# Performance work log

Measured on AMD Instinct MI355X. Metric: run time of the kernel, lower is better.

## Reference

```python
import jax, jax.numpy as jnp
import numpy as np

B, S, DIM, HEADS, MLP = 2, 2048, 1024, 16, 4096
DH = DIM // HEADS
LN_EPS = 1e-5


def layernorm(x, g, b):
    m = x.mean(-1, keepdims=True)
    v = ((x - m) ** 2).mean(-1, keepdims=True)
    return (x - m) / jnp.sqrt(v + LN_EPS) * g + b


def rope(x):
    # x: [B, H, S, dh]; interleaved-pair RoPE (rotary_embedding_torch convention)
    dh = x.shape[-1]
    s = x.shape[-2]
    inv_freq = 1.0 / (10000.0 ** (jnp.arange(0, dh, 2, dtype=jnp.float32) / dh))
    freqs = jnp.arange(s, dtype=jnp.float32)[:, None] * inv_freq[None, :]  # [S, dh/2]
    cos = jnp.repeat(jnp.cos(freqs), 2, axis=-1)  # [S, dh]
    sin = jnp.repeat(jnp.sin(freqs), 2, axis=-1)
    xp = x.reshape(x.shape[:-1] + (dh // 2, 2))
    x_rot = jnp.stack([-xp[..., 1], xp[..., 0]], axis=-1).reshape(x.shape)
    return x * cos + x_rot * sin


def setup_inputs() -> dict:
    key = jax.random.key(0)
    ks = jax.random.split(key, 10)
    w = 0.02
    return {
        "x": jax.random.normal(ks[0], (B, S, DIM), jnp.float32),
        "bias": jax.random.normal(ks[1], (B, S, S), jnp.float32) * 0.1,
        "ln1_g": jnp.ones((DIM,), jnp.float32),
        "ln1_b": jnp.zeros((DIM,), jnp.float32),
        "W_qkv": jax.random.normal(ks[2], (DIM, 3 * DIM), jnp.float32) * w,
        "W_o": jax.random.normal(ks[3], (DIM, DIM), jnp.float32) * w,
        "ln2_g": jnp.ones((DIM,), jnp.float32),
        "ln2_b": jnp.zeros((DIM,), jnp.float32),
        "W1": jax.random.normal(ks[4], (DIM, MLP), jnp.float32) * w,
        "b1": jnp.zeros((MLP,), jnp.float32),
        "W2": jax.random.normal(ks[5], (MLP, DIM), jnp.float32) * w,
        "b2": jnp.zeros((DIM,), jnp.float32),
        "pad_mask": jnp.zeros((B, S), jnp.int32),
    }


def reference(x, bias, ln1_g, ln1_b, W_qkv, W_o, ln2_g, ln2_b, W1, b1, W2, b2, pad_mask):
    b, s, d = x.shape
    h, dh = HEADS, DH
    res = x
    x1 = layernorm(x, ln1_g, ln1_b)
    qkv = (x1 @ W_qkv).reshape(b, s, h, 3 * dh)
    q, k, v = jnp.split(qkv, 3, axis=-1)            # each [B,S,H,dh]
    q = rope(q.transpose(0, 2, 1, 3))               # [B,H,S,dh]
    k = rope(k.transpose(0, 2, 1, 3))
    v = v.transpose(0, 2, 1, 3)
    scores = jnp.einsum("bhqd,bhkd->bhqk", q, k) * (dh ** -0.5)
    scores = scores + bias[:, None]                 # additive bias per batch
    key_mask = pad_mask.astype(bool)[:, None, None, :]
    scores = jnp.where(key_mask, -jnp.inf, scores)
    attn = jax.nn.softmax(scores, axis=-1)          # dropout = identity (eval)
    out = jnp.einsum("bhqk,bhkd->bhqd", attn, v)
    out = out.transpose(0, 2, 1, 3).reshape(b, s, d)
    x = res + out @ W_o
    res2 = x
    x2 = layernorm(x, ln2_g, ln2_b)
    mlp = jax.nn.gelu(x2 @ W1 + b1, approximate=False) @ W2 + b2
    return res2 + mlp
```

## Files before the change

### kernel.cpp

```cpp
#include <hip/hip_runtime.h>
#include <hip/hip_bf16.h>

#define B_   2
#define S_   2048
#define DIM_ 1024
#define H_   16
#define DH_  64
#define MLP_ 4096

typedef __bf16 bf16x8 __attribute__((ext_vector_type(8)));
typedef float  f32x4  __attribute__((ext_vector_type(4)));

__device__ __forceinline__ ushort f2bf(float f) {
    __bf16 h = (__bf16)f;
    return __builtin_bit_cast(ushort, h);
}
__device__ __forceinline__ float bf2f(ushort b) {
    union { unsigned u; float f; } x; x.u = ((unsigned)b) << 16;
    return x.f;
}

#define GLOAD_LDS16(gptr, lptr)                                                        \
    __builtin_amdgcn_global_load_lds(                                                  \
        (const __attribute__((address_space(1))) unsigned int*)(const void*)(gptr),    \
        (__attribute__((address_space(3))) unsigned int*)(void*)(lptr), 16, 0, 0)

#define MFMA_BF16(a, b, c) __builtin_amdgcn_mfma_f32_16x16x32_bf16((a), (b), (c), 0, 0, 0)

__global__ __launch_bounds__(256) void transpose_all(const float* __restrict__ Wqkv, ushort* __restrict__ Wqkvt,
                                                     const float* __restrict__ Wo,   ushort* __restrict__ Wot,
                                                     const float* __restrict__ W1,   ushort* __restrict__ W1t,
                                                     const float* __restrict__ W2,   ushort* __restrict__ W2t) {
    int id = blockIdx.x;
    const float* in; ushort* outp; int K, N, nx;
    if (id < 3072)      { in = Wqkv; outp = Wqkvt; K = 1024; N = 3072; nx = 96;  }
    else if (id < 4096) { id -= 3072; in = Wo; outp = Wot;  K = 1024; N = 1024; nx = 32;  }
    else if (id < 8192) { id -= 4096; in = W1; outp = W1t;  K = 1024; N = 4096; nx = 128; }
    else                { id -= 8192; in = W2; outp = W2t;  K = 4096; N = 1024; nx = 32;  }
    int n0 = (id % nx) * 32, k0 = (id / nx) * 32;
    __shared__ float t[32][33];
    int tx = threadIdx.x, ty = threadIdx.y;
#pragma unroll
    for (int r = 0; r < 32; r += 8)
        t[ty + r][tx] = in[(size_t)(k0 + ty + r) * N + n0 + tx];
    __syncthreads();
#pragma unroll
    for (int r = 0; r < 32; r += 8)
        outp[(size_t)(n0 + ty + r) * K + k0 + tx] = f2bf(t[tx][ty + r]);
}

__global__ __launch_bounds__(256) void ln_kernel(const float* __restrict__ in,
                                                 const float* __restrict__ g,
                                                 const float* __restrict__ beta,
                                                 ushort* __restrict__ out) {
    int row = blockIdx.x;
    float4 v = reinterpret_cast<const float4*>(in + (size_t)row * DIM_)[threadIdx.x];
    float s = v.x + v.y + v.z + v.w;
    float s2 = v.x * v.x + v.y * v.y + v.z * v.z + v.w * v.w;
#pragma unroll
    for (int m = 1; m < 64; m <<= 1) { s += __shfl_xor(s, m); s2 += __shfl_xor(s2, m); }
    __shared__ float red[8];
    int wid = threadIdx.x >> 6;
    if ((threadIdx.x & 63) == 0) { red[wid] = s; red[4 + wid] = s2; }
    __syncthreads();
    s  = red[0] + red[1] + red[2] + red[3];
    s2 = red[4] + red[5] + red[6] + red[7];
    float mean = s * (1.f / DIM_);
    float var  = s2 * (1.f / DIM_) - mean * mean;
    float inv  = rsqrtf(var + 1e-5f);
    float4 gg = reinterpret_cast<const float4*>(g)[threadIdx.x];
    float4 bb = reinterpret_cast<const float4*>(beta)[threadIdx.x];
    ushort4 o;
    o.x = f2bf((v.x - mean) * inv * gg.x + bb.x);
    o.y = f2bf((v.y - mean) * inv * gg.y + bb.y);
    o.z = f2bf((v.z - mean) * inv * gg.z + bb.z);
    o.w = f2bf((v.w - mean) * inv * gg.w + bb.w);
    reinterpret_cast<ushort4*>(out + (size_t)row * DIM_)[threadIdx.x] = o;
}

template <int RM, int RN, bool BIAS, bool GELU, bool RES, bool OBF16>
__global__ __launch_bounds__(256) void gemm_bt(const ushort* __restrict__ A,
                                               const ushort* __restrict__ Bt,
                                               void* __restrict__ Cout,
                                               const float* __restrict__ bias,
                                               const float* __restrict__ resid,
                                               int M, int N, int K) {
    constexpr int BM = RM * 64, BN = RN * 64;
    __shared__ __align__(16) ushort As[2][BM * 32];
    __shared__ __align__(16) ushort Bs[2][BN * 32];
    int tid = threadIdx.x;
    int wid = tid >> 6, lane = tid & 63;
    int lr = lane & 15, lg = lane >> 4;

    int nbx = gridDim.x;
    int nwg = nbx * gridDim.y;
    int bid = blockIdx.y * nbx + blockIdx.x;
    int swz = (bid & 7) * (nwg >> 3) + (bid >> 3);
    int row0 = (swz / nbx) * BM, col0 = (swz % nbx) * BN;

    int wm = (wid >> 1) * (RM * 32), wn = (wid & 1) * (RN * 32);
    int srow = tid >> 2, scol = (tid & 3) * 8;

    f32x4 acc[RM * 2][RN * 2] = {};

    const ushort* gA = A + (size_t)(row0 + srow) * K + scol;
    const ushort* gB = Bt + (size_t)(col0 + srow) * K + scol;

    auto stage = [&](int buf, int kt) {
#pragma unroll
        for (int r = 0; r < RM; r++)
            GLOAD_LDS16(gA + (size_t)r * 64 * K + kt, As[buf] + r * 2048 + wid * 512);
#pragma unroll
        for (int r = 0; r < RN; r++)
            GLOAD_LDS16(gB + (size_t)r * 64 * K + kt, Bs[buf] + r * 2048 + wid * 512);
    };

    int nk = K >> 5;
    stage(0, 0);
    __syncthreads();

    for (int t = 0; t < nk; t++) {
        int cur = t & 1;
        if (t + 1 < nk) stage(cur ^ 1, (t + 1) << 5);
        bf16x8 af[RM * 2], bfr[RN * 2];
#pragma unroll
        for (int m = 0; m < RM * 2; m++)
            af[m] = *reinterpret_cast<const bf16x8*>(As[cur] + (wm + m * 16 + lr) * 32 + lg * 8);
#pragma unroll
        for (int n = 0; n < RN * 2; n++)
            bfr[n] = *reinterpret_cast<const bf16x8*>(Bs[cur] + (wn + n * 16 + lr) * 32 + lg * 8);
#pragma unroll
        for (int m = 0; m < RM * 2; m++)
#pragma unroll
            for (int n = 0; n < RN * 2; n++)
                acc[m][n] = MFMA_BF16(af[m], bfr[n], acc[m][n]);
        __syncthreads();
    }

#pragma unroll
    for (int m = 0; m < RM * 2; m++) {
#pragma unroll
        for (int n = 0; n < RN * 2; n++) {
            int col = col0 + wn + n * 16 + lr;
#pragma unroll
            for (int i = 0; i < 4; i++) {
                int row = row0 + wm + m * 16 + lg * 4 + i;
                float v = acc[m][n][i];
                if (BIAS) v += bias[col];
                if (GELU) v = 0.5f * v * (1.f + erff(v * 0.70710678118f));
                if (RES)  v += resid[(size_t)row * N + col];
                if (OBF16) ((ushort*)Cout)[(size_t)row * N + col] = f2bf(v);
                else       ((float*)Cout)[(size_t)row * N + col] = v;
            }
        }
    }
}

template <bool BIAS, bool GELU, bool RES, bool OBF16>
__global__ __launch_bounds__(512) void gemm_bt512(const ushort* __restrict__ A,
                                                  const ushort* __restrict__ Bt,
                                                  void* __restrict__ Cout,
                                                  const float* __restrict__ bias,
                                                  const float* __restrict__ resid,
                                                  int M, int N, int K) {
    __shared__ __align__(16) ushort As[2][128 * 32];
    __shared__ __align__(16) ushort Bs[2][256 * 32];
    int tid = threadIdx.x;
    int wid = tid >> 6, lane = tid & 63;
    int lr = lane & 15, lg = lane >> 4;

    int nbx = gridDim.x;
    int nwg = nbx * gridDim.y;
    int bid = blockIdx.y * nbx + blockIdx.x;
    int swz = (bid & 7) * (nwg >> 3) + (bid >> 3);
    int row0 = (swz / nbx) * 128, col0 = (swz % nbx) * 256;

    int wm = (wid >> 2) * 64, wn = (wid & 3) * 64;
    int srow = tid >> 2, scol = (tid & 3) * 8;

    f32x4 acc[4][4] = {};

    const ushort* gA = A + (size_t)(row0 + srow) * K + scol;
    const ushort* gB = Bt + (size_t)(col0 + srow) * K + scol;

    auto stage = [&](int buf, int kt) {
        GLOAD_LDS16(gA + kt, As[buf] + wid * 512);
        GLOAD_LDS16(gB + kt, Bs[buf] + wid * 512);
        GLOAD_LDS16(gB + (size_t)128 * K + kt, Bs[buf] + 4096 + wid * 512);
    };

    int nk = K >> 5;
    stage(0, 0);
    __syncthreads();

    for (int t = 0; t < nk; t++) {
        int cur = t & 1;
        if (t + 1 < nk) stage(cur ^ 1, (t + 1) << 5);
        bf16x8 af[4], bfr[4];
#pragma unroll
        for (int m = 0; m < 4; m++)
            af[m] = *reinterpret_cast<const bf16x8*>(As[cur] + (wm + m * 16 + lr) * 32 + lg * 8);
#pragma unroll
        for (int n = 0; n < 4; n++)
            bfr[n] = *reinterpret_cast<const bf16x8*>(Bs[cur] + (wn + n * 16 + lr) * 32 + lg * 8);
#pragma unroll
        for (int m = 0; m < 4; m++)
#pragma unroll
            for (int n = 0; n < 4; n++)
                acc[m][n] = MFMA_BF16(af[m], bfr[n], acc[m][n]);
        __syncthreads();
    }

#pragma unroll
    for (int m = 0; m < 4; m++) {
#pragma unroll
        for (int n = 0; n < 4; n++) {
            int col = col0 + wn + n * 16 + lr;
#pragma unroll
            for (int i = 0; i < 4; i++) {
                int row = row0 + wm + m * 16 + lg * 4 + i;
                float v = acc[m][n][i];
                if (BIAS) v += bias[col];
                if (GELU) v = 0.5f * v * (1.f + erff(v * 0.70710678118f));
                if (RES)  v += resid[(size_t)row * N + col];
                if (OBF16) ((ushort*)Cout)[(size_t)row * N + col] = f2bf(v);
                else       ((float*)Cout)[(size_t)row * N + col] = v;
            }
        }
    }
}

__global__ __launch_bounds__(512) void gemm_qkv512(const ushort* __restrict__ A,
                                                   const ushort* __restrict__ Bt,
                                                   const float2* __restrict__ tab,
                                                   ushort* __restrict__ Qr,
                                                   ushort* __restrict__ Kr,
                                                   ushort* __restrict__ VT) {
    const int K = DIM_;
    __shared__ __align__(16) ushort As[2][128 * 32];
    __shared__ __align__(16) ushort Bs[2][256 * 32];
    int tid = threadIdx.x;
    int wid = tid >> 6, lane = tid & 63;
    int lr = lane & 15, lg = lane >> 4;

    int nbx = gridDim.x;
    int nwg = nbx * gridDim.y;
    int bid = blockIdx.y * nbx + blockIdx.x;
    int swz = (bid & 7) * (nwg >> 3) + (bid >> 3);
    int row0 = (swz / nbx) * 128, col0 = (swz % nbx) * 256;

    int wm = (wid >> 2) * 64, wn = (wid & 3) * 64;
    int srow = tid >> 2, scol = (tid & 3) * 8;

    f32x4 acc[4][4] = {};

    const ushort* gA = A + (size_t)(row0 + srow) * K + scol;
    const ushort* gB = Bt + (size_t)(col0 + srow) * K + scol;

    auto stage = [&](int buf, int kt) {
        GLOAD_LDS16(gA + kt, As[buf] + wid * 512);
        GLOAD_LDS16(gB + kt, Bs[buf] + wid * 512);
        GLOAD_LDS16(gB + (size_t)128 * K + kt, Bs[buf] + 4096 + wid * 512);
    };

    int nk = K >> 5;
    stage(0, 0);
    __syncthreads();

    for (int t = 0; t < nk; t++) {
        int cur = t & 1;
        if (t + 1 < nk) stage(cur ^ 1, (t + 1) << 5);
        bf16x8 af[4], bfr[4];
#pragma unroll
        for (int m = 0; m < 4; m++)
            af[m] = *reinterpret_cast<const bf16x8*>(As[cur] + (wm + m * 16 + lr) * 32 + lg * 8);
#pragma unroll
        for (int n = 0; n < 4; n++)
            bfr[n] = *reinterpret_cast<const bf16x8*>(Bs[cur] + (wn + n * 16 + lr) * 32 + lg * 8);
#pragma unroll
        for (int m = 0; m < 4; m++)
#pragma unroll
            for (int n = 0; n < 4; n++)
                acc[m][n] = MFMA_BF16(af[m], bfr[n], acc[m][n]);
        __syncthreads();
    }

#pragma unroll
    for (int n = 0; n < 4; n++) {
        int colb = col0 + wn + n * 16;
        int h    = colb / 192;
        int off  = colb % 192;
        int typ  = off >> 6;
        int d    = (off & 63) + lr;
#pragma unroll
        for (int m = 0; m < 4; m++) {
            if (typ < 2) {
                ushort* qk = (typ == 0) ? Qr : Kr;
#pragma unroll
                for (int i = 0; i < 4; i++) {
                    int row = row0 + wm + m * 16 + lg * 4 + i;
                    int b = row >> 11, s = row & (S_ - 1);
                    float v  = acc[m][n][i];
                    float pv = __shfl_xor(v, 1);
                    float2 cs = tab[(s << 5) + (d >> 1)];
                    float r = v * cs.x + ((d & 1) ? pv : -pv) * cs.y;
                    qk[((size_t)(b * H_ + h) * S_ + s) * DH_ + d] = f2bf(r);
                }
            } else {
                int row = row0 + wm + m * 16 + lg * 4;
                int b = row >> 11, s = row & (S_ - 1);
                ushort4 o4;
                o4.x = f2bf(acc[m][n][0]);
                o4.y = f2bf(acc[m][n][1]);
                o4.z = f2bf(acc[m][n][2]);
                o4.w = f2bf(acc[m][n][3]);
                *reinterpret_cast<ushort4*>(
                    VT + ((size_t)(b * H_ + h) * DH_ + d) * S_ + s) = o4;
            }
        }
    }
}

__global__ __launch_bounds__(256) void rope_table(float2* __restrict__ tab) {
    int i = blockIdx.x * 256 + threadIdx.x;
    int s = i >> 5, p = i & 31;
    float invf = __expf(-((float)(2 * p) / 64.f) * logf(10000.f));
    float a = (float)s * invf;
    tab[i] = make_float2(cosf(a), sinf(a));
}

__global__ __launch_bounds__(256) void attn_kernel(const ushort* __restrict__ Q,
                                                   const ushort* __restrict__ Kr,
                                                   const ushort* __restrict__ VT,
                                                   const float* __restrict__ bias,
                                                   const int* __restrict__ pad,
                                                   ushort* __restrict__ Out) {
    int bx = blockIdx.x;
    int qt = bx & 31, h = (bx >> 5) & 15, b = bx >> 9;
    __shared__ __align__(16) ushort Ks[64 * 72];
    __shared__ __align__(16) ushort Vs[64 * 72];
    __shared__ __align__(16) ushort Ps[64 * 72];
    int tid = threadIdx.x, wid = tid >> 6, lane = tid & 63;
    int lr = lane & 15, lg = lane >> 4;
    int q0 = qt * 64;
    const ushort* Qb = Q + ((size_t)(b * H_ + h) * S_) * DH_;
    const ushort* Kb = Kr + ((size_t)(b * H_ + h) * S_) * DH_;
    const ushort* Vb = VT + ((size_t)(b * H_ + h) * DH_) * S_;
    const float*  bb = bias + (size_t)b * S_ * S_;
    const int*    pb = pad + b * S_;

    bf16x8 qf[2];
#pragma unroll
    for (int ks = 0; ks < 2; ks++)
        qf[ks] = *reinterpret_cast<const bf16x8*>(
            Qb + (size_t)(q0 + wid * 16 + lr) * DH_ + ks * 32 + lg * 8);

    float mrow[4], lrow[4];
#pragma unroll
    for (int i = 0; i < 4; i++) { mrow[i] = -3e38f; lrow[i] = 0.f; }
    f32x4 o[4] = {};

    int sr = tid >> 3, sc = (tid & 7) * 8;
    const float scale = 0.125f;

    for (int kv0 = 0; kv0 < S_; kv0 += 64) {
        __syncthreads();
#pragma unroll
        for (int cc = 0; cc < 2; cc++) {
            int r = cc * 32 + sr;
            *reinterpret_cast<bf16x8*>(Ks + r * 72 + sc) =
                *reinterpret_cast<const bf16x8*>(Kb + (size_t)(kv0 + r) * DH_ + sc);
            *reinterpret_cast<bf16x8*>(Vs + r * 72 + sc) =
                *reinterpret_cast<const bf16x8*>(Vb + (size_t)r * S_ + kv0 + sc);
        }
        __syncthreads();

        f32x4 sa[4] = {};
#pragma unroll
        for (int n = 0; n < 4; n++) {
            bf16x8 k0 = *reinterpret_cast<const bf16x8*>(Ks + (n * 16 + lr) * 72 + lg * 8);
            bf16x8 k1 = *reinterpret_cast<const bf16x8*>(Ks + (n * 16 + lr) * 72 + 32 + lg * 8);
            sa[n] = MFMA_BF16(qf[0], k0, sa[n]);
            sa[n] = MFMA_BF16(qf[1], k1, sa[n]);
        }

        int pm[4];
#pragma unroll
        for (int n = 0; n < 4; n++) pm[n] = pb[kv0 + n * 16 + lr];

#pragma unroll
        for (int i = 0; i < 4; i++) {
            const float* brow = bb + (size_t)(q0 + wid * 16 + lg * 4 + i) * S_ + kv0;
            float sv[4];
            float rmax = -3e38f;
#pragma unroll
            for (int n = 0; n < 4; n++) {
                float s = sa[n][i] * scale + brow[n * 16 + lr];
                if (pm[n]) s = -1e30f;
                sv[n] = s;
                rmax = fmaxf(rmax, s);
            }
#pragma unroll
            for (int msk = 1; msk < 16; msk <<= 1) rmax = fmaxf(rmax, __shfl_xor(rmax, msk));
            float mnew = fmaxf(mrow[i], rmax);
            float resc = __expf(mrow[i] - mnew);
            mrow[i] = mnew;
            float ls = 0.f;
            int prow = (i << 2) | lg;
#pragma unroll
            for (int n = 0; n < 4; n++) {
                float p = __expf(sv[n] - mnew);
                ls += p;
                Ps[(wid * 16 + prow) * 72 + n * 16 + lr] = f2bf(p);
            }
            lrow[i] = lrow[i] * resc + ls;
#pragma unroll
            for (int fn = 0; fn < 4; fn++) o[fn][i] *= resc;
        }

        int plr = ((lr & 3) << 2) | (lr >> 2);
        bf16x8 pf0 = *reinterpret_cast<const bf16x8*>(Ps + (wid * 16 + plr) * 72 + lg * 8);
        bf16x8 pf1 = *reinterpret_cast<const bf16x8*>(Ps + (wid * 16 + plr) * 72 + 32 + lg * 8);

#pragma unroll
        for (int fn = 0; fn < 4; fn++) {
            bf16x8 v0 = *reinterpret_cast<const bf16x8*>(Vs + (fn * 16 + lr) * 72 + lg * 8);
            bf16x8 v1 = *reinterpret_cast<const bf16x8*>(Vs + (fn * 16 + lr) * 72 + 32 + lg * 8);
            o[fn] = MFMA_BF16(pf0, v0, o[fn]);
            o[fn] = MFMA_BF16(pf1, v1, o[fn]);
        }
    }

#pragma unroll
    for (int i = 0; i < 4; i++)
#pragma unroll
        for (int msk = 1; msk < 16; msk <<= 1) lrow[i] += __shfl_xor(lrow[i], msk);

#pragma unroll
    for (int fn = 0; fn < 4; fn++)
#pragma unroll
        for (int i = 0; i < 4; i++) {
            int qrow = q0 + wid * 16 + lg * 4 + i;
            Out[(size_t)(b * S_ + qrow) * DIM_ + h * DH_ + fn * 16 + lr] =
                f2bf(o[fn][i] / lrow[i]);
        }
}

extern "C" void kernel_launch(void* const* d_in, const int* in_sizes, int n_in,
                              void* d_out, int out_size, void* d_ws, size_t ws_size,
                              hipStream_t stream) {
    const float* x    = (const float*)d_in[0];
    const float* bias = (const float*)d_in[1];
    const float* ln1g = (const float*)d_in[2];
    const float* ln1b = (const float*)d_in[3];
    const float* Wqkv = (const float*)d_in[4];
    const float* Wo   = (const float*)d_in[5];
    const float* ln2g = (const float*)d_in[6];
    const float* ln2b = (const float*)d_in[7];
    const float* W1   = (const float*)d_in[8];
    const float* b1   = (const float*)d_in[9];
    const float* W2   = (const float*)d_in[10];
    const float* b2   = (const float*)d_in[11];
    const int*   pad  = (const int*)d_in[12];
    float* out = (float*)d_out;

    char* ws = (char*)d_ws;
    size_t off = 0;
    auto alloc = [&](size_t bytes) {
        char* p = ws + off;
        off += (bytes + 255) & ~(size_t)255;
        return (void*)p;
    };
    ushort* x1    = (ushort*)alloc((size_t)4096 * 1024 * 2);
    ushort* Wqkvt = (ushort*)alloc((size_t)3072 * 1024 * 2);
    float2* tab   = (float2*)alloc((size_t)S_ * 32 * 8);
    ushort* Qr    = (ushort*)alloc((size_t)B_ * H_ * S_ * DH_ * 2);
    ushort* Kr2   = (ushort*)alloc((size_t)B_ * H_ * S_ * DH_ * 2);
    ushort* attnO = (ushort*)alloc((size_t)4096 * 1024 * 2);
    ushort* Wot   = (ushort*)alloc((size_t)1024 * 1024 * 2);
    float*  xmid  = (float*)alloc((size_t)4096 * 1024 * 4);
    ushort* x2    = (ushort*)alloc((size_t)4096 * 1024 * 2);
    ushort* W1t   = (ushort*)alloc((size_t)4096 * 1024 * 2);
    ushort* h1    = (ushort*)alloc((size_t)4096 * 4096 * 2);
    ushort* W2t   = (ushort*)alloc((size_t)1024 * 4096 * 2);
    ushort* VT    = h1;

    dim3 tb(32, 8);
    transpose_all<<<12288, tb, 0, stream>>>(Wqkv, Wqkvt, Wo, Wot, W1, W1t, W2, W2t);

    rope_table<<<(S_ * 32) / 256, 256, 0, stream>>>(tab);

    ln_kernel<<<4096, 256, 0, stream>>>(x, ln1g, ln1b, x1);

    gemm_qkv512<<<dim3(12, 32), 512, 0, stream>>>(x1, Wqkvt, tab, Qr, Kr2, VT);

    attn_kernel<<<B_ * H_ * (S_ / 64), 256, 0, stream>>>(Qr, Kr2, VT, bias, pad, attnO);

    gemm_bt<1, 2, false, false, true, false><<<dim3(8, 64), 256, 0, stream>>>(
        attnO, Wot, xmid, nullptr, x, 4096, 1024, 1024);

    ln_kernel<<<4096, 256, 0, stream>>>(xmid, ln2g, ln2b, x2);

    gemm_bt512<true, true, false, true><<<dim3(16, 32), 512, 0, stream>>>(
        x2, W1t, h1, b1, nullptr, 4096, 4096, 1024);

    gemm_bt<1, 2, true, false, true, false><<<dim3(8, 64), 256, 0, stream>>>(
        h1, W2t, out, b2, xmid, 4096, 1024, 4096);
}
```

Baseline: 314.8 us.

## Triple-buffer GEMM LDS staging with explicit vmcnt waits and single barrier

Converts the double-buffered global-to-LDS staging in all three GEMM kernels into a three-stage ring buffer that prefetches two K-tiles ahead. Explicit s_waitcnt vmcnt waits allow later loads to stay in flight, and a single barrier per iteration replaces the trailing __syncthreads. The aim is to hide more global-load latency behind MFMA work, at the cost of more LDS per block (possible occupancy loss) and reliance on hand-counted vmcnt values. The waitcnt template only handles N of 0, 3 and 4, so the generic gemm_bt with RM+RN outside that set would emit no wait at all.

```diff
diff --git a/kernel.cpp b/kernel.cpp
--- a/kernel.cpp
+++ b/kernel.cpp
@@ -26,6 +26,16 @@
         (__attribute__((address_space(3))) unsigned int*)(void*)(lptr), 16, 0, 0)
 
 #define MFMA_BF16(a, b, c) __builtin_amdgcn_mfma_f32_16x16x32_bf16((a), (b), (c), 0, 0, 0)
+
+template <int N> __device__ __forceinline__ void waitcnt_vm() {
+    if constexpr (N == 0)      asm volatile("s_waitcnt vmcnt(0)" ::: "memory");
+    else if constexpr (N == 3) asm volatile("s_waitcnt vmcnt(3)" ::: "memory");
+    else if constexpr (N == 4) asm volatile("s_waitcnt vmcnt(4)" ::: "memory");
+}
+__device__ __forceinline__ void pipeline_barrier() {
+    __builtin_amdgcn_s_barrier();
+    asm volatile("" ::: "memory");
+}
 
 __global__ __launch_bounds__(256) void transpose_all(const float* __restrict__ Wqkv, ushort* __restrict__ Wqkvt,
                                                      const float* __restrict__ Wo,   ushort* __restrict__ Wot,
@@ -85,9 +95,9 @@
                                                const float* __restrict__ bias,
                                                const float* __restrict__ resid,
                                                int M, int N, int K) {
-    constexpr int BM = RM * 64, BN = RN * 64;
-    __shared__ __align__(16) ushort As[2][BM * 32];
-    __shared__ __align__(16) ushort Bs[2][BN * 32];
+    constexpr int BM = RM * 64, BN = RN * 64, L = RM + RN;
+    __shared__ __align__(16) ushort As[3][BM * 32];
+    __shared__ __align__(16) ushort Bs[3][BN * 32];
     int tid = threadIdx.x;
     int wid = tid >> 6, lane = tid & 63;
     int lr = lane & 15, lg = lane >> 4;
@@ -117,11 +127,14 @@
 
     int nk = K >> 5;
     stage(0, 0);
-    __syncthreads();
+    stage(1, 32);
 
     for (int t = 0; t < nk; t++) {
-        int cur = t & 1;
-        if (t + 1 < nk) stage(cur ^ 1, (t + 1) << 5);
+        int cur = t % 3;
+        if (t + 1 < nk) waitcnt_vm<L>();
+        else            waitcnt_vm<0>();
+        pipeline_barrier();
+        if (t + 2 < nk) stage((t + 2) % 3, (t + 2) << 5);
         bf16x8 af[RM * 2], bfr[RN * 2];
 #pragma unroll
         for (int m = 0; m < RM * 2; m++)
@@ -134,7 +147,6 @@
 #pragma unroll
             for (int n = 0; n < RN * 2; n++)
                 acc[m][n] = MFMA_BF16(af[m], bfr[n], acc[m][n]);
-        __syncthreads();
     }
 
 #pragma unroll
@@ -163,8 +175,8 @@
                                                   const float* __restrict__ bias,
                                                   const float* __restrict__ resid,
                                                   int M, int N, int K) {
-    __shared__ __align__(16) ushort As[2][128 * 32];
-    __shared__ __align__(16) ushort Bs[2][256 * 32];
+    __shared__ __align__(16) ushort As[3][128 * 32];
+    __shared__ __align__(16) ushort Bs[3][256 * 32];
     int tid = threadIdx.x;
     int wid = tid >> 6, lane = tid & 63;
     int lr = lane & 15, lg = lane >> 4;
@@ -191,11 +203,14 @@
 
     int nk = K >> 5;
     stage(0, 0);
-    __syncthreads();
+    stage(1, 32);
 
     for (int t = 0; t < nk; t++) {
-        int cur = t & 1;
-        if (t + 1 < nk) stage(cur ^ 1, (t + 1) << 5);
+        int cur = t % 3;
+        if (t + 1 < nk) waitcnt_vm<3>();
+        else            waitcnt_vm<0>();
+        pipeline_barrier();
+        if (t + 2 < nk) stage((t + 2) % 3, (t + 2) << 5);
         bf16x8 af[4], bfr[4];
 #pragma unroll
         for (int m = 0; m < 4; m++)
@@ -208,7 +223,6 @@
 #pragma unroll
             for (int n = 0; n < 4; n++)
                 acc[m][n] = MFMA_BF16(af[m], bfr[n], acc[m][n]);
-        __syncthreads();
     }
 
 #pragma unroll
@@ -237,8 +251,8 @@
                                                    ushort* __restrict__ Kr,
                                                    ushort* __restrict__ VT) {
     const int K = DIM_;
-    __shared__ __align__(16) ushort As[2][128 * 32];
-    __shared__ __align__(16) ushort Bs[2][256 * 32];
+    __shared__ __align__(16) ushort As[3][128 * 32];
+    __shared__ __align__(16) ushort Bs[3][256 * 32];
     int tid = threadIdx.x;
     int wid = tid >> 6, lane = tid & 63;
     int lr = lane & 15, lg = lane >> 4;
@@ -265,11 +279,14 @@
 
     int nk = K >> 5;
     stage(0, 0);
-    __syncthreads();
+    stage(1, 32);
 
     for (int t = 0; t < nk; t++) {
-        int cur = t & 1;
-        if (t + 1 < nk) stage(cur ^ 1, (t + 1) << 5);
+        int cur = t % 3;
+        if (t + 1 < nk) waitcnt_vm<3>();
+        else            waitcnt_vm<0>();
+        pipeline_barrier();
+        if (t + 2 < nk) stage((t + 2) % 3, (t + 2) << 5);
         bf16x8 af[4], bfr[4];
 #pragma unroll
         for (int m = 0; m < 4; m++)
@@ -282,7 +299,6 @@
 #pragma unroll
             for (int n = 0; n < 4; n++)
                 acc[m][n] = MFMA_BF16(af[m], bfr[n], acc[m][n]);
-        __syncthreads();
     }
 
 #pragma unroll
```

Measured after the change: 342.2 us. 8.7% more time.
